# Optimization experiments

Hardware: AMD Instinct MI355X
Metric: run time of the kernel (lower is better)

Reference implementation:

```python
import jax, jax.numpy as jnp
import numpy as np

B_SZ, L, D, N = 2, 2048, 1024, 16


def setup_inputs() -> dict:
    key = jax.random.key(0)
    ks = jax.random.split(key, 8)
    x = jax.random.normal(ks[0], (B_SZ, L, D), dtype=jnp.float32)
    # torch.nn.Linear params: weight [out, in], bias [out]; y = x @ W.T + b
    s1 = 1.0 / np.sqrt(D)
    W1 = jax.random.uniform(ks[1], (D, D), minval=-s1, maxval=s1, dtype=jnp.float32)
    b1 = jax.random.uniform(ks[2], (D,), minval=-s1, maxval=s1, dtype=jnp.float32)
    W2 = jax.random.uniform(ks[3], (N, D), minval=-s1, maxval=s1, dtype=jnp.float32)
    b2 = jax.random.uniform(ks[4], (N,), minval=-s1, maxval=s1, dtype=jnp.float32)
    W3 = jax.random.uniform(ks[5], (N, D), minval=-s1, maxval=s1, dtype=jnp.float32)
    b3 = jax.random.uniform(ks[6], (N,), minval=-s1, maxval=s1, dtype=jnp.float32)
    # A: xavier_uniform on (D, N)
    lim = np.sqrt(6.0 / (D + N))
    A = jax.random.uniform(ks[7], (D, N), minval=-lim, maxval=lim, dtype=jnp.float32)
    return {"x": x, "W1": W1, "b1": b1, "W2": W2, "b2": b2, "W3": W3, "b3": b3, "A": A}


def reference(x, W1, b1, W2, b2, W3, b3, A):
    # delta = softplus(fc1(x)); B = fc2(x); C = fc3(x)
    delta = jax.nn.softplus(x @ W1.T + b1)          # [b, l, d]
    Bm = x @ W2.T + b2                               # [b, l, n]
    Cm = x @ W3.T + b3                               # [b, l, n]
    # discretization: dB = einsum('bld,bln->bldn', delta, B)
    dB = jnp.einsum('bld,bln->bldn', delta, Bm)      # [b, l, d, n]
    # dA = exp(einsum('bld,dn->bldn', delta, A)) is computed in the source but
    # multiplies a zero-initialized h, so it does not affect the output.
    # h = dA*0 + x[..., None] * dB
    h = x[..., None] * dB                            # [b, l, d, n]
    y = jnp.einsum('bln,bldn->bld', Cm, h)           # [b, l, d]
    return y
```

## Files before the change

### kernel.cpp

```cpp
#include <hip/hip_runtime.h>
#include <hip/hip_bf16.h>
#include <math.h>


typedef __bf16 bf16x8 __attribute__((ext_vector_type(8)));
typedef __bf16 bf16x4 __attribute__((ext_vector_type(4)));
typedef float  f32x4  __attribute__((ext_vector_type(4)));

#define MDIM 4096
#define KDIM 1024
#define NDIM 1024

__device__ __forceinline__ void async16(const void* g, void* l) {
    __builtin_amdgcn_global_load_lds(
        (const __attribute__((address_space(1))) void*)g,
        (__attribute__((address_space(3))) void*)l, 16, 0, 0);
}

__device__ __forceinline__ float softplus_f(float z) {
    return fmaxf(z, 0.f) + log1pf(__expf(-fabsf(z)));
}

#define NX4 ((MDIM * KDIM) / 4)
#define NW4 ((KDIM * NDIM) / 4)
#define NC4 ((32 * KDIM) / 4)
__global__ __launch_bounds__(256)
void convert_kernel(const float* __restrict__ x, const float* __restrict__ W1,
                    const float* __restrict__ W2, const float* __restrict__ W3,
                    __bf16* __restrict__ xb, __bf16* __restrict__ w1b,
                    __bf16* __restrict__ wcb) {
    const size_t i = (size_t)blockIdx.x * 256 + threadIdx.x;
    if (i < NX4) {
        float4 v = reinterpret_cast<const float4*>(x)[i];
        bf16x4 h = { (__bf16)v.x, (__bf16)v.y, (__bf16)v.z, (__bf16)v.w };
        reinterpret_cast<bf16x4*>(xb)[i] = h;
    } else if (i < NX4 + NW4) {
        const size_t j = i - NX4;
        float4 v = reinterpret_cast<const float4*>(W1)[j];
        bf16x4 h = { (__bf16)v.x, (__bf16)v.y, (__bf16)v.z, (__bf16)v.w };
        reinterpret_cast<bf16x4*>(w1b)[j] = h;
    } else {
        const size_t j = i - NX4 - NW4;
        if (j < NC4) {
            const int row = (int)(j >> 8);
            const int c4  = (int)(j & 255);
            const float* __restrict__ src = (row < 16)
                ? (W2 + (size_t)row * KDIM) : (W3 + (size_t)(row - 16) * KDIM);
            float4 v = reinterpret_cast<const float4*>(src)[c4];
            bf16x4 h = { (__bf16)v.x, (__bf16)v.y, (__bf16)v.z, (__bf16)v.w };
            reinterpret_cast<bf16x4*>(wcb)[row * 256 + c4] = h;
        }
    }
}
#define CONV_GRID ((NX4 + NW4 + NC4) / 256)

__global__ __launch_bounds__(256)
void s_mfma(const __bf16* __restrict__ xb, const __bf16* __restrict__ wcb,
            const float* __restrict__ b2, const float* __restrict__ b3,
            float* __restrict__ s) {
    __shared__ __align__(16) __bf16 xs[16 * 1032];
    __shared__ float red[4][2][16][16];
    const int t = threadIdx.x;
    const int wave = t >> 6, lane = t & 63;
    const int lrow = lane & 15, quad = lane >> 4;
    const size_t m0 = (size_t)blockIdx.x * 16;
    const int wk0 = wave * 256;

#pragma unroll
    for (int i = 0; i < 8; ++i) {
        const int idx = i * 256 + t;
        const int row = idx >> 7;
        const int c8  = (idx & 127) * 8;
        bf16x8 v = *reinterpret_cast<const bf16x8*>(xb + (m0 + row) * KDIM + c8);
        *reinterpret_cast<bf16x8*>(&xs[row * 1032 + c8]) = v;
    }
    __syncthreads();

    f32x4 acc[2] = {};
#pragma unroll
    for (int ks = 0; ks < 256; ks += 32) {
        bf16x8 a = *reinterpret_cast<const bf16x8*>(
            &xs[lrow * 1032 + wk0 + ks + quad * 8]);
        bf16x8 b0 = *reinterpret_cast<const bf16x8*>(
            wcb + (size_t)lrow * KDIM + wk0 + ks + quad * 8);
        acc[0] = __builtin_amdgcn_mfma_f32_16x16x32_bf16(a, b0, acc[0], 0, 0, 0);
        bf16x8 b1 = *reinterpret_cast<const bf16x8*>(
            wcb + (size_t)(16 + lrow) * KDIM + wk0 + ks + quad * 8);
        acc[1] = __builtin_amdgcn_mfma_f32_16x16x32_bf16(a, b1, acc[1], 0, 0, 0);
    }
#pragma unroll
    for (int r = 0; r < 4; ++r) {
        red[wave][0][quad * 4 + r][lrow] = acc[0][r];
        red[wave][1][quad * 4 + r][lrow] = acc[1][r];
    }
    __syncthreads();

    {
        const int row = t >> 4, n = t & 15;
        float Bv = red[0][0][row][n] + red[1][0][row][n]
                 + red[2][0][row][n] + red[3][0][row][n] + b2[n];
        float Cv = red[0][1][row][n] + red[1][1][row][n]
                 + red[2][1][row][n] + red[3][1][row][n] + b3[n];
        float p = Bv * Cv;
        p += __shfl_xor(p, 1);
        p += __shfl_xor(p, 2);
        p += __shfl_xor(p, 4);
        p += __shfl_xor(p, 8);
        if (n == 0) s[m0 + row] = p;
    }
}

#define GBM 64
#define GBN 64
#define GBK 64
__global__ __launch_bounds__(256, 4)
void gemm_bf(const __bf16* __restrict__ xb, const __bf16* __restrict__ w1b,
             const float* __restrict__ x, const float* __restrict__ b1,
             const float* __restrict__ s, float* __restrict__ y) {
    __shared__ __align__(16) __bf16 As[GBM * GBK];
    __shared__ __align__(16) __bf16 Bs[GBN * GBK];
    const int bm = blockIdx.y, bn = blockIdx.x;
    const int t = threadIdx.x;
    const int wave = t >> 6, lane = t & 63;
    const int wm = (wave >> 1) * 32, wn = (wave & 1) * 32;
    const int lrow = lane & 15, quad = lane >> 4;
    const int srow = lane >> 3;
    const int scol = ((lane & 7) ^ srow) * 8;
    const size_t m0 = (size_t)bm * GBM, n0 = (size_t)bn * GBN;

    f32x4 acc[2][2] = {};

    for (int k0 = 0; k0 < KDIM; k0 += GBK) {
#pragma unroll
        for (int i = 0; i < 2; ++i) {
            int q = wave * 2 + i; int row = 8 * q + srow;
            async16(xb + (m0 + row) * KDIM + k0 + scol, &As[q * 512]);
            async16(w1b + (n0 + row) * KDIM + k0 + scol, &Bs[q * 512]);
        }
        __syncthreads();

#pragma unroll
        for (int kk = 0; kk < GBK; kk += 32) {
            const int cg = (kk >> 3) + quad;
            bf16x8 af[2], bfr[2];
#pragma unroll
            for (int mi = 0; mi < 2; ++mi) {
                int row = wm + mi * 16 + lrow;
                af[mi] = *reinterpret_cast<const bf16x8*>(
                    &As[row * GBK + ((cg ^ (row & 7)) << 3)]);
            }
#pragma unroll
            for (int ni = 0; ni < 2; ++ni) {
                int row = wn + ni * 16 + lrow;
                bfr[ni] = *reinterpret_cast<const bf16x8*>(
                    &Bs[row * GBK + ((cg ^ (row & 7)) << 3)]);
            }
#pragma unroll
            for (int mi = 0; mi < 2; ++mi)
#pragma unroll
                for (int ni = 0; ni < 2; ++ni)
                    acc[mi][ni] = __builtin_amdgcn_mfma_f32_16x16x32_bf16(
                        af[mi], bfr[ni], acc[mi][ni], 0, 0, 0);
        }
        __syncthreads();
    }

#pragma unroll
    for (int ni = 0; ni < 2; ++ni) {
        const size_t gn = n0 + wn + ni * 16 + lrow;
        const float bias = b1[gn];
#pragma unroll
        for (int mi = 0; mi < 2; ++mi) {
#pragma unroll
            for (int r = 0; r < 4; ++r) {
                const size_t gm = m0 + wm + mi * 16 + quad * 4 + r;
                float z = acc[mi][ni][r] + bias;
                y[gm * NDIM + gn] = x[gm * NDIM + gn] * softplus_f(z) * s[gm];
            }
        }
    }
}

__global__ __launch_bounds__(256)
void s_kernel_fb(const float* __restrict__ x,
                 const float* __restrict__ W2, const float* __restrict__ b2,
                 const float* __restrict__ W3, const float* __restrict__ b3,
                 float* __restrict__ s) {
    __shared__ float xs[1024];
    __shared__ float ps[8][32];
    __shared__ float bc[32];
    const int m = blockIdx.x;
    const int t = threadIdx.x;
    reinterpret_cast<float4*>(xs)[t] =
        reinterpret_cast<const float4*>(x + (size_t)m * 1024)[t];
    __syncthreads();
    const int n = t & 15;
    const int mat = (t >> 4) & 1;
    const int seg = t >> 5;
    const float* __restrict__ W = mat ? W3 : W2;
    const float* __restrict__ wr = W + (size_t)n * 1024 + seg * 128;
    const float* __restrict__ xr = xs + seg * 128;
    float p = 0.f;
#pragma unroll
    for (int i = 0; i < 128; i += 4) {
        float4 w4 = *reinterpret_cast<const float4*>(wr + i);
        float4 x4 = *reinterpret_cast<const float4*>(xr + i);
        p += w4.x * x4.x + w4.y * x4.y + w4.z * x4.z + w4.w * x4.w;
    }
    ps[seg][t & 31] = p;
    __syncthreads();
    if (t < 32) {
        float tot = 0.f;
#pragma unroll
        for (int g = 0; g < 8; ++g) tot += ps[g][t];
        tot += (t < 16) ? b2[t] : b3[t - 16];
        bc[t] = tot;
    }
    __syncthreads();
    if (t == 0) {
        float ss = 0.f;
#pragma unroll
        for (int nn = 0; nn < 16; ++nn) ss += bc[nn] * bc[16 + nn];
        s[m] = ss;
    }
}

#define BM 128
#define BN 64
#define BK 64
#define LDK 72
__global__ __launch_bounds__(256)
void gemm_fused_fb(const float* __restrict__ x, const float* __restrict__ W1,
                   const float* __restrict__ b1, const float* __restrict__ s,
                   float* __restrict__ y) {
    __shared__ __align__(16) __bf16 As[BM * LDK];
    __shared__ __align__(16) __bf16 Bs[BN * LDK];
    const int bm = blockIdx.y;
    const int bn = blockIdx.x;
    const int t = threadIdx.x;
    const int wave = t >> 6;
    const int lane = t & 63;
    const int wm = (wave >> 1) * 64;
    const int wn = (wave & 1) * 32;
    const int lrow = lane & 15;
    const int quad = lane >> 4;
    f32x4 acc[4][2] = {};
    const int rbase = t >> 4;
    const int scol = (t & 15) * 4;
    const float* __restrict__ xg = x + (size_t)(bm * BM) * KDIM + scol;
    const float* __restrict__ wg = W1 + (size_t)(bn * BN) * KDIM + scol;
    for (int k0 = 0; k0 < KDIM; k0 += BK) {
#pragma unroll
        for (int rr = 0; rr < 8; ++rr) {
            int row = rr * 16 + rbase;
            float4 v = *reinterpret_cast<const float4*>(xg + (size_t)row * KDIM + k0);
            bf16x4 h = { (__bf16)v.x, (__bf16)v.y, (__bf16)v.z, (__bf16)v.w };
            *reinterpret_cast<bf16x4*>(&As[row * LDK + scol]) = h;
        }
#pragma unroll
        for (int rr = 0; rr < 4; ++rr) {
            int row = rr * 16 + rbase;
            float4 v = *reinterpret_cast<const float4*>(wg + (size_t)row * KDIM + k0);
            bf16x4 h = { (__bf16)v.x, (__bf16)v.y, (__bf16)v.z, (__bf16)v.w };
            *reinterpret_cast<bf16x4*>(&Bs[row * LDK + scol]) = h;
        }
        __syncthreads();
#pragma unroll
        for (int kk = 0; kk < BK; kk += 32) {
            bf16x8 af[4];
            bf16x8 bfr[2];
#pragma unroll
            for (int mi = 0; mi < 4; ++mi)
                af[mi] = *reinterpret_cast<const bf16x8*>(
                    &As[(wm + mi * 16 + lrow) * LDK + kk + quad * 8]);
#pragma unroll
            for (int ni = 0; ni < 2; ++ni)
                bfr[ni] = *reinterpret_cast<const bf16x8*>(
                    &Bs[(wn + ni * 16 + lrow) * LDK + kk + quad * 8]);
#pragma unroll
            for (int mi = 0; mi < 4; ++mi)
#pragma unroll
                for (int ni = 0; ni < 2; ++ni)
                    acc[mi][ni] = __builtin_amdgcn_mfma_f32_16x16x32_bf16(
                        af[mi], bfr[ni], acc[mi][ni], 0, 0, 0);
        }
        __syncthreads();
    }
    const int gmb = bm * BM + wm;
    const int gnb = bn * BN + wn;
#pragma unroll
    for (int ni = 0; ni < 2; ++ni) {
        const int gn = gnb + ni * 16 + lrow;
        const float bias = b1[gn];
#pragma unroll
        for (int mi = 0; mi < 4; ++mi) {
            const int gm0 = gmb + mi * 16 + quad * 4;
#pragma unroll
            for (int r = 0; r < 4; ++r) {
                const int gm = gm0 + r;
                float z = acc[mi][ni][r] + bias;
                y[(size_t)gm * NDIM + gn] =
                    x[(size_t)gm * NDIM + gn] * softplus_f(z) * s[gm];
            }
        }
    }
}

extern "C" void kernel_launch(void* const* d_in, const int* in_sizes, int n_in,
                              void* d_out, int out_size, void* d_ws, size_t ws_size,
                              hipStream_t stream) {
    const float* x  = (const float*)d_in[0];
    const float* W1 = (const float*)d_in[1];
    const float* b1 = (const float*)d_in[2];
    const float* W2 = (const float*)d_in[3];
    const float* b2 = (const float*)d_in[4];
    const float* W3 = (const float*)d_in[5];
    const float* b3 = (const float*)d_in[6];

    float* y = (float*)d_out;

    const size_t XB_BYTES = (size_t)MDIM * KDIM * 2;
    const size_t WB_BYTES = (size_t)NDIM * KDIM * 2;
    const size_t WC_BYTES = (size_t)32 * KDIM * 2;
    const size_t S_BYTES  = (size_t)MDIM * 4;

    if (ws_size >= XB_BYTES + WB_BYTES + WC_BYTES + S_BYTES) {
        __bf16* xb  = (__bf16*)d_ws;
        __bf16* w1b = (__bf16*)((char*)d_ws + XB_BYTES);
        __bf16* wcb = (__bf16*)((char*)d_ws + XB_BYTES + WB_BYTES);
        float*  s   = (float*)((char*)d_ws + XB_BYTES + WB_BYTES + WC_BYTES);
        convert_kernel<<<dim3(CONV_GRID), dim3(256), 0, stream>>>(
            x, W1, W2, W3, xb, w1b, wcb);
        s_mfma<<<dim3(MDIM / 16), dim3(256), 0, stream>>>(xb, wcb, b2, b3, s);
        gemm_bf<<<dim3(NDIM / GBN, MDIM / GBM), dim3(256), 0, stream>>>(
            xb, w1b, x, b1, s, y);
    } else {
        float* s = (float*)d_ws;
        s_kernel_fb<<<dim3(MDIM), dim3(256), 0, stream>>>(x, W2, b2, W3, b3, s);
        gemm_fused_fb<<<dim3(NDIM / BN, MDIM / BM), dim3(256), 0, stream>>>(x, W1, b1, s, y);
    }
}
```

Baseline: 112.5 us.

## Replace 4-wave GEMM block with single-wave double-buffered 64x64 tile kernel

```diff
diff --git a/kernel.cpp b/kernel.cpp
--- a/kernel.cpp
+++ b/kernel.cpp
@@ -113,67 +113,77 @@
 #define GBM 64
 #define GBN 64
 #define GBK 64
-__global__ __launch_bounds__(256, 4)
-void gemm_bf(const __bf16* __restrict__ xb, const __bf16* __restrict__ w1b,
-             const float* __restrict__ x, const float* __restrict__ b1,
-             const float* __restrict__ s, float* __restrict__ y) {
-    __shared__ __align__(16) __bf16 As[GBM * GBK];
-    __shared__ __align__(16) __bf16 Bs[GBN * GBK];
-    const int bm = blockIdx.y, bn = blockIdx.x;
-    const int t = threadIdx.x;
-    const int wave = t >> 6, lane = t & 63;
-    const int wm = (wave >> 1) * 32, wn = (wave & 1) * 32;
+#define NIT (KDIM / GBK)
+__global__ __launch_bounds__(64)
+void gemm_wave(const __bf16* __restrict__ xb, const __bf16* __restrict__ w1b,
+               const float* __restrict__ x, const float* __restrict__ b1,
+               const float* __restrict__ s, float* __restrict__ y) {
+    __shared__ __align__(16) __bf16 As[2][GBM * GBK];
+    __shared__ __align__(16) __bf16 Bs[2][GBN * GBK];
+    const int bm = blockIdx.x, bn = blockIdx.y;
+    const int lane = threadIdx.x;
     const int lrow = lane & 15, quad = lane >> 4;
     const int srow = lane >> 3;
     const int scol = ((lane & 7) ^ srow) * 8;
     const size_t m0 = (size_t)bm * GBM, n0 = (size_t)bn * GBN;
 
-    f32x4 acc[2][2] = {};
-
-    for (int k0 = 0; k0 < KDIM; k0 += GBK) {
-#pragma unroll
-        for (int i = 0; i < 2; ++i) {
-            int q = wave * 2 + i; int row = 8 * q + srow;
-            async16(xb + (m0 + row) * KDIM + k0 + scol, &As[q * 512]);
-            async16(w1b + (n0 + row) * KDIM + k0 + scol, &Bs[q * 512]);
-        }
+    f32x4 acc[4][4] = {};
+
+#pragma unroll
+    for (int q = 0; q < 8; ++q) {
+        int row = q * 8 + srow;
+        async16(xb + (m0 + row) * KDIM + scol, &As[0][q * 512]);
+        async16(w1b + (n0 + row) * KDIM + scol, &Bs[0][q * 512]);
+    }
+
+    for (int it = 0; it < NIT; ++it) {
+        const int p = it & 1;
         __syncthreads();
+
+        if (it + 1 < NIT) {
+            const int k1 = (it + 1) * GBK;
+#pragma unroll
+            for (int q = 0; q < 8; ++q) {
+                int row = q * 8 + srow;
+                async16(xb + (m0 + row) * KDIM + k1 + scol, &As[p ^ 1][q * 512]);
+                async16(w1b + (n0 + row) * KDIM + k1 + scol, &Bs[p ^ 1][q * 512]);
+            }
+        }
 
 #pragma unroll
         for (int kk = 0; kk < GBK; kk += 32) {
             const int cg = (kk >> 3) + quad;
-            bf16x8 af[2], bfr[2];
-#pragma unroll
-            for (int mi = 0; mi < 2; ++mi) {
-                int row = wm + mi * 16 + lrow;
+            bf16x8 af[4], bfr[4];
+#pragma unroll
+            for (int mi = 0; mi < 4; ++mi) {
+                int row = mi * 16 + lrow;
                 af[mi] = *reinterpret_cast<const bf16x8*>(
-                    &As[row * GBK + ((cg ^ (row & 7)) << 3)]);
-            }
-#pragma unroll
-            for (int ni = 0; ni < 2; ++ni) {
-                int row = wn + ni * 16 + lrow;
+                    &As[p][row * GBK + ((cg ^ (row & 7)) << 3)]);
+            }
+#pragma unroll
+            for (int ni = 0; ni < 4; ++ni) {
+                int row = ni * 16 + lrow;
                 bfr[ni] = *reinterpret_cast<const bf16x8*>(
-                    &Bs[row * GBK + ((cg ^ (row & 7)) << 3)]);
-            }
-#pragma unroll
-            for (int mi = 0; mi < 2; ++mi)
-#pragma unroll
-                for (int ni = 0; ni < 2; ++ni)
+                    &Bs[p][row * GBK + ((cg ^ (row & 7)) << 3)]);
+            }
+#pragma unroll
+            for (int mi = 0; mi < 4; ++mi)
+#pragma unroll
+                for (int ni = 0; ni < 4; ++ni)
                     acc[mi][ni] = __builtin_amdgcn_mfma_f32_16x16x32_bf16(
                         af[mi], bfr[ni], acc[mi][ni], 0, 0, 0);
         }
-        __syncthreads();
-    }
-
-#pragma unroll
-    for (int ni = 0; ni < 2; ++ni) {
-        const size_t gn = n0 + wn + ni * 16 + lrow;
+    }
+
+#pragma unroll
+    for (int ni = 0; ni < 4; ++ni) {
+        const size_t gn = n0 + ni * 16 + lrow;
         const float bias = b1[gn];
 #pragma unroll
-        for (int mi = 0; mi < 2; ++mi) {
+        for (int mi = 0; mi < 4; ++mi) {
 #pragma unroll
             for (int r = 0; r < 4; ++r) {
-                const size_t gm = m0 + wm + mi * 16 + quad * 4 + r;
+                const size_t gm = m0 + mi * 16 + quad * 4 + r;
                 float z = acc[mi][ni][r] + bias;
                 y[gm * NDIM + gn] = x[gm * NDIM + gn] * softplus_f(z) * s[gm];
             }
@@ -332,7 +342,7 @@
         convert_kernel<<<dim3(CONV_GRID), dim3(256), 0, stream>>>(
             x, W1, W2, W3, xb, w1b, wcb);
         s_mfma<<<dim3(MDIM / 16), dim3(256), 0, stream>>>(xb, wcb, b2, b3, s);
-        gemm_bf<<<dim3(NDIM / GBN, MDIM / GBM), dim3(256), 0, stream>>>(
+        gemm_wave<<<dim3(MDIM / GBM, NDIM / GBN), dim3(64), 0, stream>>>(
             xb, w1b, x, b1, s, y);
     } else {
         float* s = (float*)d_ws;
```

Measured after the change: 130.1 us. 1.16x slower.
